# Kernel tuning notes

Hardware: AMD Instinct MI355X
Metric: run time of the kernel (lower is better)

Reference implementation:

```python
import jax, jax.numpy as jnp
import numpy as np

NQ = 11          # qubits per atom
NL = 3           # circuit layers (and message-passing layers)
S = 2 ** NQ      # statevector size
PAD = 100        # feature-map input width


def setup_inputs() -> dict:
    key = jax.random.key(0)
    ks = jax.random.split(key, 18)
    B, A, F, E = 8, 96, 64, 384
    return {
        "node_features": jax.random.normal(ks[0], (B, A, F), jnp.float32),
        "edge_indices": jax.random.randint(ks[1], (2, E), 0, A),
        # QuantumFeatureMap.feature_preprocessor: Linear(100,64) -> ReLU -> Linear(64,NQ) -> Tanh
        "W1": jax.random.normal(ks[2], (64, PAD), jnp.float32) * 0.1,
        "b1": jnp.zeros((64,), jnp.float32),
        "W2": jax.random.normal(ks[3], (NQ, 64), jnp.float32) * 0.1,
        "b2": jnp.zeros((NQ,), jnp.float32),
        # QuantumFeatureMap circuit params
        "rot": jax.random.normal(ks[4], (NL, NQ, 3), jnp.float32),
        "ent": jax.random.normal(ks[5], (NL, NQ - 1), jnp.float32),
        # one QuantumMessagePassing layer per NL, each with message_gates [NQ,3]
        "msg_gates": jax.random.normal(ks[6], (NL, NQ, 3), jnp.float32),
        # QuantumGlobalPooling
        "pool_w": jax.random.normal(ks[7], (NQ,), jnp.float32),
        # output MLP: Linear(2*NQ,256)->ReLU->Linear(256,128)->ReLU->Linear(128,64)
        "Wo1": jax.random.normal(ks[8], (256, 2 * NQ), jnp.float32) * 0.1,
        "bo1": jnp.zeros((256,), jnp.float32),
        "Wo2": jax.random.normal(ks[9], (128, 256), jnp.float32) * 0.05,
        "bo2": jnp.zeros((128,), jnp.float32),
        "Wo3": jax.random.normal(ks[10], (64, 128), jnp.float32) * 0.05,
        "bo3": jnp.zeros((64,), jnp.float32),
    }


def _apply_rotation(amps, M, q):
    """Apply per-batch 2x2 gate M [N,2,2] on qubit q of amps [N,S]."""
    N = amps.shape[0]
    lo = 1 << q
    hi = S // (2 * lo)
    a = amps.reshape(N, hi, 2, lo)  # bit q of state index is the middle axis
    return jnp.einsum('nij,nhjl->nhil', M, a).reshape(N, S)


def _forward(node_features, W1, b1, W2, b2, rot, ent, msg_gates, pool_w,
             Wo1, bo1, Wo2, bo2, Wo3, bo3):
    B, A, F = node_features.shape
    N = B * A
    # --- QuantumNodeEmbedding: pad atom features to 100, shared feature map ---
    x = node_features.reshape(N, F)
    x = jnp.pad(x, ((0, 0), (0, PAD - F)))
    h = jax.nn.relu(x @ W1.T + b1)
    f = jnp.tanh(h @ W2.T + b2)            # [N, NQ] per-qubit angles scaling
    amps = jnp.zeros((N, S), jnp.complex64).at[:, 0].set(1.0)
    states = jnp.arange(S)
    # --- QuantumFeatureMap circuit ---
    for l in range(NL):
        for q in range(NQ):
            rx = rot[l, q, 0] * f[:, q]
            ry = rot[l, q, 1] * f[:, q]
            rz = rot[l, q, 2] * f[:, q]
            cx, sx = jnp.cos(rx / 2), jnp.sin(rx / 2)
            cy, sy = jnp.cos(ry / 2), jnp.sin(ry / 2)
            cz, sz = jnp.cos(rz / 2), jnp.sin(rz / 2)
            # rotation matrix exactly as in the torch source
            M = jnp.stack([cx * cy * cz, -sx * sy * sz,
                           sx * sy * cz,  cx * cy * sz], -1)
            M = M.reshape(N, 2, 2).astype(jnp.complex64)
            amps = _apply_rotation(amps, M, q)
        for q in range(NQ - 1):
            # parameterized CNOT: for control-bit==1, mix state with target-flipped partner
            p = jax.nn.sigmoid(ent[l, q]).astype(jnp.complex64)
            ctrl = (states >> q) & 1
            partner = states ^ (1 << (q + 1))
            mixed = (1 - p) * amps + p * amps[:, partner]
            amps = jnp.where(ctrl[None, :] == 1, mixed, amps)
    # --- QuantumMessagePassing layers: diagonal phase exp(i*sum(theta_q over set bits)) ---
    bits = ((states[:, None] >> jnp.arange(NQ)[None, :]) & 1).astype(jnp.float32)  # [S,NQ]
    for l in range(NL):
        theta = msg_gates[l].sum(-1)                 # [NQ] rx+ry+rz per qubit
        phase = jnp.exp(1j * (bits @ theta))         # [S] complex64
        amps = amps * phase[None, :]
    # --- QuantumGlobalPooling ---
    amps_b = amps.reshape(B, A, S)
    w = jax.nn.sigmoid(pool_w[jnp.arange(A) % NQ]).astype(jnp.complex64)  # atom i -> w[i%NQ]
    pooled = jnp.einsum('a,bas->bs', w, amps_b)      # [B,S] complex
    norm = jnp.sqrt(jnp.sum(pooled.real ** 2 + pooled.imag ** 2, axis=1, keepdims=True))
    pooled = pooled / jnp.maximum(norm, 1e-12)
    rm = jnp.tile(pooled.real.mean(1, keepdims=True), (1, NQ))
    im = jnp.tile(pooled.imag.mean(1, keepdims=True), (1, NQ))
    rep = jnp.concatenate([rm, im], axis=1)          # [B, 2*NQ]
    # --- output network ---
    h1 = jax.nn.relu(rep @ Wo1.T + bo1)
    h2 = jax.nn.relu(h1 @ Wo2.T + bo2)
    return h2 @ Wo3.T + bo3                          # [B, 64]


def reference(node_features, edge_indices, W1, b1, W2, b2, rot, ent, msg_gates,
              pool_w, Wo1, bo1, Wo2, bo2, Wo3, bo3):
    # edge_indices is accepted by the torch module but does not enter the math
    del edge_indices
    return _forward(node_features, W1, b1, W2, b2, rot, ent, msg_gates, pool_w,
                    Wo1, bo1, Wo2, bo2, Wo3, bo3)
```

## Files before the change

kernel.cpp:

```cpp
#include <hip/hip_runtime.h>

#define NQ 11
#define NL 3
#define S  2048
#define NB 8
#define NA 96
#define NF 64
#define PADW 100
#define WPB 4
#define PPB (NA / WPB)

typedef float v2f __attribute__((ext_vector_type(2)));

#if defined(__has_builtin)
#if __has_builtin(__builtin_amdgcn_permlane16_swap) && __has_builtin(__builtin_amdgcn_permlane32_swap)
#define USE_PLSWAP 1
#endif
#endif
#ifndef USE_PLSWAP
#define USE_PLSWAP 0
#endif

__device__ __forceinline__ float sigmoidf_(float x) { return 1.0f / (1.0f + expf(-x)); }

__device__ __forceinline__ float rl_(float v, int srclane) {
    return __builtin_bit_cast(float, __builtin_amdgcn_readlane(__builtin_bit_cast(int, v), srclane));
}

template<int M> __device__ __forceinline__ float dpp_x(float x) {
    const int xi = __builtin_bit_cast(int, x);
    if constexpr (M == 1)
        return __builtin_bit_cast(float, __builtin_amdgcn_mov_dpp(xi, 0xB1, 0xF, 0xF, true));
    else if constexpr (M == 2)
        return __builtin_bit_cast(float, __builtin_amdgcn_mov_dpp(xi, 0x4E, 0xF, 0xF, true));
    else {
        static_assert(M == 8, "dpp_x: unsupported mask");
        return __builtin_bit_cast(float, __builtin_amdgcn_mov_dpp(xi, 0x128, 0xF, 0xF, true));
    }
}

__device__ __forceinline__ float dppcnd4_(float x, int lane) {
    const int xi = __builtin_bit_cast(int, x);
    const int a  = __builtin_amdgcn_mov_dpp(xi, 0x104, 0xF, 0xF, true);
    const int b  = __builtin_amdgcn_mov_dpp(xi, 0x114, 0xF, 0xF, true);
    return __builtin_bit_cast(float, (lane & 4) ? b : a);
}

template<int M> __device__ __forceinline__ void lohi_fast(float x, float& lo, float& hi) {
#if USE_PLSWAP
    const unsigned xi = __builtin_bit_cast(unsigned, x);
    if constexpr (M == 16) {
        auto p = __builtin_amdgcn_permlane16_swap(xi, xi, false, false);
        lo = __builtin_bit_cast(float, p[0]); hi = __builtin_bit_cast(float, p[1]);
    } else {
        static_assert(M == 32, "lohi_fast: unsupported mask");
        auto p = __builtin_amdgcn_permlane32_swap(xi, xi, false, false);
        lo = __builtin_bit_cast(float, p[0]); hi = __builtin_bit_cast(float, p[1]);
    }
#else
    float pw;
    int lane_ = threadIdx.x & 63;
    if constexpr (M == 16)
        pw = __builtin_bit_cast(float, __builtin_amdgcn_ds_swizzle(__builtin_bit_cast(int, x), 0x401F));
    else
        pw = __shfl_xor(x, 32, 64);
    const bool b = (lane_ & M) != 0;
    lo = b ? pw : x;
    hi = b ? x : pw;
#endif
}

template<bool FAST, int M> __device__ __forceinline__ float pxf(float x, int lane) {
    if constexpr (M == 1 || M == 2 || M == 8) {
        (void)lane; return dpp_x<M>(x);
    } else if constexpr (M == 4) {
        if constexpr (FAST) { return dppcnd4_(x, lane); }
        else { (void)lane; return __builtin_bit_cast(float,
                 __builtin_amdgcn_ds_swizzle(__builtin_bit_cast(int, x), 0x101F)); }
    } else if constexpr (M == 16) {
        if constexpr (FAST) {
            float lo, hi; lohi_fast<16>(x, lo, hi);
            return ((lane >> 4) & 1) ? lo : hi;
        } else { (void)lane; return __builtin_bit_cast(float,
                 __builtin_amdgcn_ds_swizzle(__builtin_bit_cast(int, x), 0x401F)); }
    } else {
        static_assert(M == 32, "pxf: unsupported mask");
        if constexpr (FAST) {
            float lo, hi; lohi_fast<32>(x, lo, hi);
            return ((lane >> 5) & 1) ? lo : hi;
        } else { (void)lane; return __shfl_xor(x, 32, 64); }
    }
}
template<bool FAST, int M> __device__ __forceinline__ v2f pxv(v2f w, int lane) {
    v2f r; r.x = pxf<FAST, M>(w.x, lane); r.y = pxf<FAST, M>(w.y, lane); return r;
}

template<bool FAST, int Q> __device__ __forceinline__ void rot_lane(v2f* w, float g00, float g01,
                                                                    float g10, float g11, int lane) {
    const int bit  = (lane >> Q) & 1;
    const float c1 = bit ? g11 : g00;
    const float c0 = bit ? g10 : g01;
    v2f pw[16];
#pragma unroll
    for (int j = 0; j < 16; ++j) pw[j] = pxv<FAST, (1 << Q)>(w[j], lane);
#pragma unroll
    for (int j = 0; j < 16; ++j) w[j] = c1 * w[j] + c0 * pw[j];
}
__device__ __forceinline__ void rot_comp(v2f* w, float g00, float g01, float g10, float g11) {
    v2f ca; ca.x = g00; ca.y = g11;
    v2f cb; cb.x = g01; cb.y = g10;
#pragma unroll
    for (int j = 0; j < 16; ++j) {
        v2f sw; sw.x = w[j].y; sw.y = w[j].x;
        w[j] = ca * w[j] + cb * sw;
    }
}
template<int B> __device__ __forceinline__ void rot_reg(v2f* w, float g00, float g01,
                                                        float g10, float g11) {
#pragma unroll
    for (int t = 0; t < 8; ++t) {
        const int j0 = ((t >> B) << (B + 1)) | (t & ((1 << B) - 1));
        const int j1 = j0 | (1 << B);
        v2f a0 = w[j0], a1 = w[j1];
        w[j0] = g00 * a0 + g01 * a1;
        w[j1] = g10 * a0 + g11 * a1;
    }
}
template<bool FAST, int Q> __device__ __forceinline__ void ent_lane(v2f* w, float p, int lane) {
    const float pact = p * (float)((lane >> Q) & 1);
    v2f pw[16];
#pragma unroll
    for (int j = 0; j < 16; ++j) pw[j] = pxv<FAST, (1 << (Q + 1))>(w[j], lane);
#pragma unroll
    for (int j = 0; j < 16; ++j) w[j] = w[j] + pact * (pw[j] - w[j]);
}
__device__ __forceinline__ void ent_5(v2f* w, float p, int lane) {
    const float pact = p * (float)((lane >> 5) & 1);
#pragma unroll
    for (int j = 0; j < 16; ++j) {
        v2f sw; sw.x = w[j].y; sw.y = w[j].x;
        w[j] = w[j] + pact * (sw - w[j]);
    }
}
__device__ __forceinline__ void ent_6(v2f* w, float p) {
#pragma unroll
    for (int t = 0; t < 8; ++t) {
        const int j0 = 2 * t, j1 = 2 * t + 1;
        const float d = w[j1].y - w[j0].y;
        w[j0].y = fmaf(p, d, w[j0].y);
        w[j1].y = fmaf(-p, d, w[j1].y);
    }
}
template<int B> __device__ __forceinline__ void ent_reg(v2f* w, float p) {
#pragma unroll
    for (int t = 0; t < 4; ++t) {
        const int j0 = ((t >> B) << (B + 2)) | (1 << B) | (t & ((1 << B) - 1));
        const int j1 = j0 | (1 << (B + 1));
        v2f d = w[j1] - w[j0];
        w[j0] = w[j0] + p * d;
        w[j1] = w[j1] - p * d;
    }
}

template<bool FAST> __device__ __forceinline__ void gates_run(v2f* w, float m00, float m01,
                                                              float m10, float m11, float pent,
                                                              int lane) {
#define GC(G) const int gi = gb + (G); \
    const float g00 = rl_(m00, gi), g01 = rl_(m01, gi), g10 = rl_(m10, gi), g11 = rl_(m11, gi)
#define ROTL(Q) { GC(Q); rot_lane<FAST, Q>(w, g00, g01, g10, g11, lane); }
#define ROTR(B) { GC((B) + 7); rot_reg<B>(w, g00, g01, g10, g11); }
#define ENTL(Q) { const float p = rl_(pent, eb + (Q)); ent_lane<FAST, Q>(w, p, lane); }
#pragma clang loop unroll(disable)
    for (int l = 0; l < NL; ++l) {
        const int gb = l * NQ;
        const int eb = l * (NQ - 1);
        ROTL(0) ROTL(1) ROTL(2) ROTL(3) ROTL(4) ROTL(5)
        { GC(6); rot_comp(w, g00, g01, g10, g11); }
        ROTR(0) ROTR(1) ROTR(2) ROTR(3)
        ENTL(0) ENTL(1) ENTL(2) ENTL(3) ENTL(4)
        { const float p = rl_(pent, eb + 5); ent_5(w, p, lane); }
        { const float p = rl_(pent, eb + 6); ent_6(w, p); }
        { const float p = rl_(pent, eb + 7); ent_reg<0>(w, p); }
        { const float p = rl_(pent, eb + 8); ent_reg<1>(w, p); }
        { const float p = rl_(pent, eb + 9); ent_reg<2>(w, p); }
    }
#undef GC
#undef ROTL
#undef ROTR
#undef ENTL
}

__global__ __launch_bounds__(256) void circuit_kernel(
    const float* __restrict__ nf,
    const float* __restrict__ W1,
    const float* __restrict__ b1,
    const float* __restrict__ W2,
    const float* __restrict__ b2,
    const float* __restrict__ rot,
    const float* __restrict__ ent,
    const float* __restrict__ pool_w,
    float* __restrict__ Rpart)
{
    __shared__ float W1s[64 * 65];
    __shared__ float xs[WPB][64];
    __shared__ float psum[WPB][S];

    const int tid  = threadIdx.x;
    const int lane = tid & 63;
    const int wave = tid >> 6;
    const int node = blockIdx.x * WPB + wave;
    const int a    = node % NA;

    {
        const int r  = tid >> 2;
        const int c0 = (tid & 3) << 4;
        const float4* src = reinterpret_cast<const float4*>(W1 + r * PADW + c0);
        float* dst = &W1s[r * 65 + c0];
#pragma unroll
        for (int j = 0; j < 4; ++j) {
            const float4 vv = src[j];
            dst[4 * j + 0] = vv.x; dst[4 * j + 1] = vv.y;
            dst[4 * j + 2] = vv.z; dst[4 * j + 3] = vv.w;
        }
        xs[wave][lane] = nf[blockIdx.x * (WPB * NF) + tid];
    }

    float w2v[NQ];
#pragma unroll
    for (int q = 0; q < NQ; ++q) w2v[q] = W2[q * 64 + lane];
    const float b2l = b2[lane < NQ ? lane : 0];

    bool okf;
    {
        const float idf = __builtin_bit_cast(float, lane);
        bool ok = (__builtin_bit_cast(int, dppcnd4_(idf, lane)) == (lane ^ 4));
        float lo, hi;
        lohi_fast<16>(idf, lo, hi);
        ok = ok && (__builtin_bit_cast(int, lo) == (lane & ~16))
                && (__builtin_bit_cast(int, hi) == (lane | 16));
        lohi_fast<32>(idf, lo, hi);
        ok = ok && (__builtin_bit_cast(int, lo) == (lane & ~32))
                && (__builtin_bit_cast(int, hi) == (lane | 32));
        okf = __all(ok);
    }
    __syncthreads();

    float h = b1[lane];
    {
        const float* wrow = &W1s[lane * 65];
        const float* xv   = xs[wave];
#pragma unroll
        for (int k = 0; k < 64; ++k) h = fmaf(wrow[k], xv[k], h);
    }
    h = fmaxf(h, 0.0f);

    float t[NQ];
#pragma unroll
    for (int q = 0; q < NQ; ++q) t[q] = h * w2v[q];
#pragma unroll
    for (int off = 32; off >= 1; off >>= 1) {
#pragma unroll
        for (int q = 0; q < NQ; ++q) t[q] += __shfl_xor(t[q], off, 64);
    }
    float fscal = 0.0f;
#pragma unroll
    for (int q = 0; q < NQ; ++q) if (lane == q) fscal = tanhf(t[q] + b2l);

    const int qidx = lane < 11 ? lane : (lane < 22 ? lane - 11 : (lane < 33 ? lane - 22 : 0));
    const float fg = __shfl(fscal, qidx, 64);
    float m00 = 0.f, m01 = 0.f, m10 = 0.f, m11 = 0.f;
    if (lane < NL * NQ) {
        const float* r = rot + lane * 3;
        const float hx = 0.5f * r[0] * fg;
        const float hy = 0.5f * r[1] * fg;
        const float hz = 0.5f * r[2] * fg;
        const float cx = cosf(hx), sx = sinf(hx);
        const float cy = cosf(hy), sy = sinf(hy);
        const float cz = cosf(hz), sz = sinf(hz);
        m00 = cx * cy * cz; m01 = -sx * sy * sz;
        m10 = sx * sy * cz; m11 = cx * cy * sz;
    }
    float pent = 0.0f;
    if (lane < NL * (NQ - 1)) pent = sigmoidf_(ent[lane]);

    v2f w[16];
#pragma unroll
    for (int j = 0; j < 16; ++j) { w[j].x = 0.0f; w[j].y = 0.0f; }
    if (lane == 0) w[0].x = 1.0f;

    if (okf) gates_run<true >(w, m00, m01, m10, m11, pent, lane);
    else     gates_run<false>(w, m00, m01, m10, m11, pent, lane);

    const float wgt = sigmoidf_(pool_w[a % NQ]);
#pragma unroll
    for (int j = 0; j < 16; ++j) {
        psum[wave][((2 * j + 0) << 6) | lane] = wgt * w[j].x;
        psum[wave][((2 * j + 1) << 6) | lane] = wgt * w[j].y;
    }
    __syncthreads();
    {
        float* Rb = Rpart + (size_t)blockIdx.x * S;
        for (int s = tid; s < S; s += 256)
            Rb[s] = psum[0][s] + psum[1][s] + psum[2][s] + psum[3][s];
    }
}

__global__ __launch_bounds__(512) void pool_mlp_kernel(
    const float* __restrict__ Rpart,
    const float* __restrict__ msg,
    const float* __restrict__ Wo1, const float* __restrict__ bo1,
    const float* __restrict__ Wo2, const float* __restrict__ bo2,
    const float* __restrict__ Wo3, const float* __restrict__ bo3,
    float* __restrict__ out)
{
    __shared__ float Theta[NQ];
    __shared__ float red[3][8];
    __shared__ float rm_sh, im_sh;
    __shared__ float h1[256];
    __shared__ float h2[128];

    const int b   = blockIdx.x;
    const int tid = threadIdx.x;

    if (tid < NQ) {
        float t = 0.0f;
        for (int l = 0; l < NL; ++l)
#pragma unroll
            for (int c = 0; c < 3; ++c) t += msg[(l * NQ + tid) * 3 + c];
        Theta[tid] = t;
    }
    __syncthreads();

    float psq = 0.0f, pc = 0.0f, ps = 0.0f;
    {
        const float4* Pb = reinterpret_cast<const float4*>(Rpart + (size_t)b * PPB * S);
        float4 R; R.x = 0.f; R.y = 0.f; R.z = 0.f; R.w = 0.f;
#pragma unroll 6
        for (int j = 0; j < PPB; ++j) {
            const float4 v = Pb[j * (S / 4) + tid];
            R.x += v.x; R.y += v.y; R.z += v.z; R.w += v.w;
        }
        const int s0 = tid * 4;
        float phiH = 0.0f;
#pragma unroll
        for (int q = 2; q < NQ; ++q)
            if ((s0 >> q) & 1) phiH += Theta[q];
        const float t0 = Theta[0], t1 = Theta[1];
        const float ph0 = phiH, ph1 = phiH + t0, ph2 = phiH + t1, ph3 = phiH + t0 + t1;
        psq = R.x * R.x + R.y * R.y + R.z * R.z + R.w * R.w;
        pc  = R.x * cosf(ph0) + R.y * cosf(ph1) + R.z * cosf(ph2) + R.w * cosf(ph3);
        ps  = R.x * sinf(ph0) + R.y * sinf(ph1) + R.z * sinf(ph2) + R.w * sinf(ph3);
    }
#pragma unroll
    for (int off = 32; off >= 1; off >>= 1) {
        psq += __shfl_xor(psq, off, 64);
        pc  += __shfl_xor(pc,  off, 64);
        ps  += __shfl_xor(ps,  off, 64);
    }
    const int lane = tid & 63, wave = tid >> 6;
    if (lane == 0) { red[0][wave] = psq; red[1][wave] = pc; red[2][wave] = ps; }
    __syncthreads();
    if (tid == 0) {
        float sq = 0.f, sc = 0.f, ss = 0.f;
#pragma unroll
        for (int wv = 0; wv < 8; ++wv) { sq += red[0][wv]; sc += red[1][wv]; ss += red[2][wv]; }
        const float norm = fmaxf(sqrtf(sq), 1e-12f);
        rm_sh = sc / (float)S / norm;
        im_sh = ss / (float)S / norm;
    }
    __syncthreads();
    const float rm = rm_sh, im = im_sh;

    if (tid < 256) {
        float s1 = 0.0f, s2 = 0.0f;
        const float* wrow = Wo1 + tid * (2 * NQ);
#pragma unroll
        for (int k = 0; k < NQ; ++k)       s1 += wrow[k];
#pragma unroll
        for (int k = NQ; k < 2 * NQ; ++k)  s2 += wrow[k];
        h1[tid] = fmaxf(rm * s1 + im * s2 + bo1[tid], 0.0f);
    }
    __syncthreads();
    if (tid < 128) {
        float acc = bo2[tid];
        const float* wrow = Wo2 + tid * 256;
        for (int k = 0; k < 256; ++k) acc += h1[k] * wrow[k];
        h2[tid] = fmaxf(acc, 0.0f);
    }
    __syncthreads();
    if (tid < 64) {
        float acc = bo3[tid];
        const float* wrow = Wo3 + tid * 128;
        for (int k = 0; k < 128; ++k) acc += h2[k] * wrow[k];
        out[b * 64 + tid] = acc;
    }
}

extern "C" void kernel_launch(void* const* d_in, const int* in_sizes, int n_in,
                              void* d_out, int out_size, void* d_ws, size_t ws_size,
                              hipStream_t stream) {
    const float* nf     = (const float*)d_in[0];
    const float* W1     = (const float*)d_in[2];
    const float* b1     = (const float*)d_in[3];
    const float* W2     = (const float*)d_in[4];
    const float* b2     = (const float*)d_in[5];
    const float* rot    = (const float*)d_in[6];
    const float* ent    = (const float*)d_in[7];
    const float* msg    = (const float*)d_in[8];
    const float* pool_w = (const float*)d_in[9];
    const float* Wo1    = (const float*)d_in[10];
    const float* bo1    = (const float*)d_in[11];
    const float* Wo2    = (const float*)d_in[12];
    const float* bo2    = (const float*)d_in[13];
    const float* Wo3    = (const float*)d_in[14];
    const float* bo3    = (const float*)d_in[15];

    float* Rpart = (float*)d_ws;

    circuit_kernel<<<dim3(NB * NA / WPB), dim3(256), 0, stream>>>(
        nf, W1, b1, W2, b2, rot, ent, pool_w, Rpart);

    pool_mlp_kernel<<<dim3(NB), dim3(512), 0, stream>>>(
        Rpart, msg, Wo1, bo1, Wo2, bo2, Wo3, bo3, (float*)d_out);
}
```

Baseline: 112.7 us.

## Simulate two atoms' statevectors per wave to raise per-wave ILP

Each wave now evolves two node statevectors at once, holding 32 complex pairs per lane instead of 16, so the grid halves to 96 blocks of 8 nodes. Gate coefficient readlanes and cross-lane permutes are interleaved over twice as many independent registers, which is meant to hide shuffle and FMA latency and amortise per-gate overhead. The costs are higher register pressure (launch bounds now set min blocks to 1), fewer waves in flight across the device, and a larger LDS reduction buffer per block.

```diff
diff --git a/kernel.cpp b/kernel.cpp
--- a/kernel.cpp
+++ b/kernel.cpp
@@ -8,7 +8,9 @@
 #define NF 64
 #define PADW 100
 #define WPB 4
-#define PPB (NA / WPB)
+#define NPW 2
+#define NPB (WPB * NPW)
+#define PPB (NA / NPB)
 
 typedef float v2f __attribute__((ext_vector_type(2)));
 
@@ -95,66 +97,80 @@
     v2f r; r.x = pxf<FAST, M>(w.x, lane); r.y = pxf<FAST, M>(w.y, lane); return r;
 }
 
-template<bool FAST, int Q> __device__ __forceinline__ void rot_lane(v2f* w, float g00, float g01,
-                                                                    float g10, float g11, int lane) {
-    const int bit  = (lane >> Q) & 1;
-    const float c1 = bit ? g11 : g00;
-    const float c0 = bit ? g10 : g01;
-    v2f pw[16];
-#pragma unroll
-    for (int j = 0; j < 16; ++j) pw[j] = pxv<FAST, (1 << Q)>(w[j], lane);
-#pragma unroll
-    for (int j = 0; j < 16; ++j) w[j] = c1 * w[j] + c0 * pw[j];
-}
-__device__ __forceinline__ void rot_comp(v2f* w, float g00, float g01, float g10, float g11) {
-    v2f ca; ca.x = g00; ca.y = g11;
-    v2f cb; cb.x = g01; cb.y = g10;
-#pragma unroll
-    for (int j = 0; j < 16; ++j) {
+template<bool FAST, int Q> __device__ __forceinline__ void rot_lane2(
+    v2f* w, float gA00, float gA01, float gA10, float gA11,
+            float gB00, float gB01, float gB10, float gB11, int lane) {
+    const int bit   = (lane >> Q) & 1;
+    const float cA1 = bit ? gA11 : gA00, cA0 = bit ? gA10 : gA01;
+    const float cB1 = bit ? gB11 : gB00, cB0 = bit ? gB10 : gB01;
+    v2f pw[32];
+#pragma unroll
+    for (int j = 0; j < 32; ++j) pw[j] = pxv<FAST, (1 << Q)>(w[j], lane);
+#pragma unroll
+    for (int j = 0; j < 32; ++j) {
+        const float c1 = (j < 16) ? cA1 : cB1;
+        const float c0 = (j < 16) ? cA0 : cB0;
+        w[j] = c1 * w[j] + c0 * pw[j];
+    }
+}
+__device__ __forceinline__ void rot_comp2(
+    v2f* w, float gA00, float gA01, float gA10, float gA11,
+            float gB00, float gB01, float gB10, float gB11) {
+    v2f caA; caA.x = gA00; caA.y = gA11;
+    v2f cbA; cbA.x = gA01; cbA.y = gA10;
+    v2f caB; caB.x = gB00; caB.y = gB11;
+    v2f cbB; cbB.x = gB01; cbB.y = gB10;
+#pragma unroll
+    for (int j = 0; j < 32; ++j) {
         v2f sw; sw.x = w[j].y; sw.y = w[j].x;
-        w[j] = ca * w[j] + cb * sw;
-    }
-}
-template<int B> __device__ __forceinline__ void rot_reg(v2f* w, float g00, float g01,
-                                                        float g10, float g11) {
-#pragma unroll
-    for (int t = 0; t < 8; ++t) {
-        const int j0 = ((t >> B) << (B + 1)) | (t & ((1 << B) - 1));
+        w[j] = ((j < 16) ? caA : caB) * w[j] + ((j < 16) ? cbA : cbB) * sw;
+    }
+}
+template<int B> __device__ __forceinline__ void rot_reg2(
+    v2f* w, float gA00, float gA01, float gA10, float gA11,
+            float gB00, float gB01, float gB10, float gB11) {
+#pragma unroll
+    for (int t = 0; t < 16; ++t) {
+        const int half = t >> 3, tt = t & 7;
+        const int j0 = (((tt >> B) << (B + 1)) | (tt & ((1 << B) - 1))) | (half << 4);
         const int j1 = j0 | (1 << B);
+        const float g00 = half ? gB00 : gA00, g01 = half ? gB01 : gA01;
+        const float g10 = half ? gB10 : gA10, g11 = half ? gB11 : gA11;
         v2f a0 = w[j0], a1 = w[j1];
         w[j0] = g00 * a0 + g01 * a1;
         w[j1] = g10 * a0 + g11 * a1;
     }
 }
-template<bool FAST, int Q> __device__ __forceinline__ void ent_lane(v2f* w, float p, int lane) {
+template<bool FAST, int Q> __device__ __forceinline__ void ent_lane2(v2f* w, float p, int lane) {
     const float pact = p * (float)((lane >> Q) & 1);
-    v2f pw[16];
-#pragma unroll
-    for (int j = 0; j < 16; ++j) pw[j] = pxv<FAST, (1 << (Q + 1))>(w[j], lane);
-#pragma unroll
-    for (int j = 0; j < 16; ++j) w[j] = w[j] + pact * (pw[j] - w[j]);
-}
-__device__ __forceinline__ void ent_5(v2f* w, float p, int lane) {
+    v2f pw[32];
+#pragma unroll
+    for (int j = 0; j < 32; ++j) pw[j] = pxv<FAST, (1 << (Q + 1))>(w[j], lane);
+#pragma unroll
+    for (int j = 0; j < 32; ++j) w[j] = w[j] + pact * (pw[j] - w[j]);
+}
+__device__ __forceinline__ void ent_5_2(v2f* w, float p, int lane) {
     const float pact = p * (float)((lane >> 5) & 1);
 #pragma unroll
-    for (int j = 0; j < 16; ++j) {
+    for (int j = 0; j < 32; ++j) {
         v2f sw; sw.x = w[j].y; sw.y = w[j].x;
         w[j] = w[j] + pact * (sw - w[j]);
     }
 }
-__device__ __forceinline__ void ent_6(v2f* w, float p) {
-#pragma unroll
-    for (int t = 0; t < 8; ++t) {
+__device__ __forceinline__ void ent_6_2(v2f* w, float p) {
+#pragma unroll
+    for (int t = 0; t < 16; ++t) {
         const int j0 = 2 * t, j1 = 2 * t + 1;
         const float d = w[j1].y - w[j0].y;
         w[j0].y = fmaf(p, d, w[j0].y);
         w[j1].y = fmaf(-p, d, w[j1].y);
     }
 }
-template<int B> __device__ __forceinline__ void ent_reg(v2f* w, float p) {
-#pragma unroll
-    for (int t = 0; t < 4; ++t) {
-        const int j0 = ((t >> B) << (B + 2)) | (1 << B) | (t & ((1 << B) - 1));
+template<int B> __device__ __forceinline__ void ent_reg2(v2f* w, float p) {
+#pragma unroll
+    for (int t = 0; t < 8; ++t) {
+        const int half = t >> 2, tt = t & 3;
+        const int j0 = ((((tt >> B) << (B + 2)) | (1 << B) | (tt & ((1 << B) - 1)))) | (half << 4);
         const int j1 = j0 | (1 << (B + 1));
         v2f d = w[j1] - w[j0];
         w[j0] = w[j0] + p * d;
@@ -162,35 +178,36 @@
     }
 }
 
-template<bool FAST> __device__ __forceinline__ void gates_run(v2f* w, float m00, float m01,
-                                                              float m10, float m11, float pent,
-                                                              int lane) {
-#define GC(G) const int gi = gb + (G); \
-    const float g00 = rl_(m00, gi), g01 = rl_(m01, gi), g10 = rl_(m10, gi), g11 = rl_(m11, gi)
-#define ROTL(Q) { GC(Q); rot_lane<FAST, Q>(w, g00, g01, g10, g11, lane); }
-#define ROTR(B) { GC((B) + 7); rot_reg<B>(w, g00, g01, g10, g11); }
-#define ENTL(Q) { const float p = rl_(pent, eb + (Q)); ent_lane<FAST, Q>(w, p, lane); }
+template<bool FAST> __device__ __forceinline__ void gates_run2(
+    v2f* w, float mA00, float mA01, float mA10, float mA11,
+            float mB00, float mB01, float mB10, float mB11, float pent, int lane) {
+#define GC2(G) const int gi = gb + (G); \
+    const float gA00 = rl_(mA00, gi), gA01 = rl_(mA01, gi), gA10 = rl_(mA10, gi), gA11 = rl_(mA11, gi); \
+    const float gB00 = rl_(mB00, gi), gB01 = rl_(mB01, gi), gB10 = rl_(mB10, gi), gB11 = rl_(mB11, gi)
+#define ROTL2(Q) { GC2(Q); rot_lane2<FAST, Q>(w, gA00, gA01, gA10, gA11, gB00, gB01, gB10, gB11, lane); }
+#define ROTR2(B) { GC2((B) + 7); rot_reg2<B>(w, gA00, gA01, gA10, gA11, gB00, gB01, gB10, gB11); }
+#define ENTL2(Q) { const float p = rl_(pent, eb + (Q)); ent_lane2<FAST, Q>(w, p, lane); }
 #pragma clang loop unroll(disable)
     for (int l = 0; l < NL; ++l) {
         const int gb = l * NQ;
         const int eb = l * (NQ - 1);
-        ROTL(0) ROTL(1) ROTL(2) ROTL(3) ROTL(4) ROTL(5)
-        { GC(6); rot_comp(w, g00, g01, g10, g11); }
-        ROTR(0) ROTR(1) ROTR(2) ROTR(3)
-        ENTL(0) ENTL(1) ENTL(2) ENTL(3) ENTL(4)
-        { const float p = rl_(pent, eb + 5); ent_5(w, p, lane); }
-        { const float p = rl_(pent, eb + 6); ent_6(w, p); }
-        { const float p = rl_(pent, eb + 7); ent_reg<0>(w, p); }
-        { const float p = rl_(pent, eb + 8); ent_reg<1>(w, p); }
-        { const float p = rl_(pent, eb + 9); ent_reg<2>(w, p); }
-    }
-#undef GC
-#undef ROTL
-#undef ROTR
-#undef ENTL
-}
-
-__global__ __launch_bounds__(256) void circuit_kernel(
+        ROTL2(0) ROTL2(1) ROTL2(2) ROTL2(3) ROTL2(4) ROTL2(5)
+        { GC2(6); rot_comp2(w, gA00, gA01, gA10, gA11, gB00, gB01, gB10, gB11); }
+        ROTR2(0) ROTR2(1) ROTR2(2) ROTR2(3)
+        ENTL2(0) ENTL2(1) ENTL2(2) ENTL2(3) ENTL2(4)
+        { const float p = rl_(pent, eb + 5); ent_5_2(w, p, lane); }
+        { const float p = rl_(pent, eb + 6); ent_6_2(w, p); }
+        { const float p = rl_(pent, eb + 7); ent_reg2<0>(w, p); }
+        { const float p = rl_(pent, eb + 8); ent_reg2<1>(w, p); }
+        { const float p = rl_(pent, eb + 9); ent_reg2<2>(w, p); }
+    }
+#undef GC2
+#undef ROTL2
+#undef ROTR2
+#undef ENTL2
+}
+
+__global__ __launch_bounds__(256, 1) void circuit_kernel(
     const float* __restrict__ nf,
     const float* __restrict__ W1,
     const float* __restrict__ b1,
@@ -202,14 +219,15 @@
     float* __restrict__ Rpart)
 {
     __shared__ float W1s[64 * 65];
-    __shared__ float xs[WPB][64];
-    __shared__ float psum[WPB][S];
+    __shared__ float xs[NPB][64];
+    __shared__ float psum[NPB][S];
 
     const int tid  = threadIdx.x;
     const int lane = tid & 63;
     const int wave = tid >> 6;
-    const int node = blockIdx.x * WPB + wave;
-    const int a    = node % NA;
+    const int nodeA = blockIdx.x * NPB + 2 * wave;
+    const int aA    = nodeA % NA;
+    const int aB    = (nodeA + 1) % NA;
 
     {
         const int r  = tid >> 2;
@@ -222,7 +240,10 @@
             dst[4 * j + 0] = vv.x; dst[4 * j + 1] = vv.y;
             dst[4 * j + 2] = vv.z; dst[4 * j + 3] = vv.w;
         }
-        xs[wave][lane] = nf[blockIdx.x * (WPB * NF) + tid];
+        float* xsf = &xs[0][0];
+        const int base = blockIdx.x * (NPB * NF);
+        xsf[tid]       = nf[base + tid];
+        xsf[tid + 256] = nf[base + tid + 256];
     }
 
     float w2v[NQ];
@@ -245,63 +266,91 @@
     }
     __syncthreads();
 
-    float h = b1[lane];
+    float hA = b1[lane], hB = hA;
     {
         const float* wrow = &W1s[lane * 65];
-        const float* xv   = xs[wave];
-#pragma unroll
-        for (int k = 0; k < 64; ++k) h = fmaf(wrow[k], xv[k], h);
-    }
-    h = fmaxf(h, 0.0f);
-
-    float t[NQ];
-#pragma unroll
-    for (int q = 0; q < NQ; ++q) t[q] = h * w2v[q];
+        const float* xvA  = xs[2 * wave];
+        const float* xvB  = xs[2 * wave + 1];
+#pragma unroll
+        for (int k = 0; k < 64; ++k) {
+            hA = fmaf(wrow[k], xvA[k], hA);
+            hB = fmaf(wrow[k], xvB[k], hB);
+        }
+    }
+    hA = fmaxf(hA, 0.0f);
+    hB = fmaxf(hB, 0.0f);
+
+    float tA[NQ], tB[NQ];
+#pragma unroll
+    for (int q = 0; q < NQ; ++q) { tA[q] = hA * w2v[q]; tB[q] = hB * w2v[q]; }
 #pragma unroll
     for (int off = 32; off >= 1; off >>= 1) {
 #pragma unroll
-        for (int q = 0; q < NQ; ++q) t[q] += __shfl_xor(t[q], off, 64);
-    }
-    float fscal = 0.0f;
-#pragma unroll
-    for (int q = 0; q < NQ; ++q) if (lane == q) fscal = tanhf(t[q] + b2l);
+        for (int q = 0; q < NQ; ++q) {
+            tA[q] += __shfl_xor(tA[q], off, 64);
+            tB[q] += __shfl_xor(tB[q], off, 64);
+        }
+    }
+    float fscalA = 0.0f, fscalB = 0.0f;
+#pragma unroll
+    for (int q = 0; q < NQ; ++q) {
+        if (lane == q) { fscalA = tanhf(tA[q] + b2l); fscalB = tanhf(tB[q] + b2l); }
+    }
 
     const int qidx = lane < 11 ? lane : (lane < 22 ? lane - 11 : (lane < 33 ? lane - 22 : 0));
-    const float fg = __shfl(fscal, qidx, 64);
-    float m00 = 0.f, m01 = 0.f, m10 = 0.f, m11 = 0.f;
+    const float fgA = __shfl(fscalA, qidx, 64);
+    const float fgB = __shfl(fscalB, qidx, 64);
+    float mA00 = 0.f, mA01 = 0.f, mA10 = 0.f, mA11 = 0.f;
+    float mB00 = 0.f, mB01 = 0.f, mB10 = 0.f, mB11 = 0.f;
     if (lane < NL * NQ) {
         const float* r = rot + lane * 3;
-        const float hx = 0.5f * r[0] * fg;
-        const float hy = 0.5f * r[1] * fg;
-        const float hz = 0.5f * r[2] * fg;
-        const float cx = cosf(hx), sx = sinf(hx);
-        const float cy = cosf(hy), sy = sinf(hy);
-        const float cz = cosf(hz), sz = sinf(hz);
-        m00 = cx * cy * cz; m01 = -sx * sy * sz;
-        m10 = sx * sy * cz; m11 = cx * cy * sz;
+        const float r0 = r[0], r1 = r[1], r2 = r[2];
+        {
+            const float hx = 0.5f * r0 * fgA, hy = 0.5f * r1 * fgA, hz = 0.5f * r2 * fgA;
+            const float cx = cosf(hx), sx = sinf(hx);
+            const float cy = cosf(hy), sy = sinf(hy);
+            const float cz = cosf(hz), sz = sinf(hz);
+            mA00 = cx * cy * cz; mA01 = -sx * sy * sz;
+            mA10 = sx * sy * cz; mA11 = cx * cy * sz;
+        }
+        {
+            const float hx = 0.5f * r0 * fgB, hy = 0.5f * r1 * fgB, hz = 0.5f * r2 * fgB;
+            const float cx = cosf(hx), sx = sinf(hx);
+            const float cy = cosf(hy), sy = sinf(hy);
+            const float cz = cosf(hz), sz = sinf(hz);
+            mB00 = cx * cy * cz; mB01 = -sx * sy * sz;
+            mB10 = sx * sy * cz; mB11 = cx * cy * sz;
+        }
     }
     float pent = 0.0f;
     if (lane < NL * (NQ - 1)) pent = sigmoidf_(ent[lane]);
 
-    v2f w[16];
-#pragma unroll
-    for (int j = 0; j < 16; ++j) { w[j].x = 0.0f; w[j].y = 0.0f; }
-    if (lane == 0) w[0].x = 1.0f;
-
-    if (okf) gates_run<true >(w, m00, m01, m10, m11, pent, lane);
-    else     gates_run<false>(w, m00, m01, m10, m11, pent, lane);
-
-    const float wgt = sigmoidf_(pool_w[a % NQ]);
+    v2f w[32];
+#pragma unroll
+    for (int j = 0; j < 32; ++j) { w[j].x = 0.0f; w[j].y = 0.0f; }
+    if (lane == 0) { w[0].x = 1.0f; w[16].x = 1.0f; }
+
+    if (okf) gates_run2<true >(w, mA00, mA01, mA10, mA11, mB00, mB01, mB10, mB11, pent, lane);
+    else     gates_run2<false>(w, mA00, mA01, mA10, mA11, mB00, mB01, mB10, mB11, pent, lane);
+
+    const float wgtA = sigmoidf_(pool_w[aA % NQ]);
+    const float wgtB = sigmoidf_(pool_w[aB % NQ]);
 #pragma unroll
     for (int j = 0; j < 16; ++j) {
-        psum[wave][((2 * j + 0) << 6) | lane] = wgt * w[j].x;
-        psum[wave][((2 * j + 1) << 6) | lane] = wgt * w[j].y;
+        psum[2 * wave + 0][((2 * j + 0) << 6) | lane] = wgtA * w[j].x;
+        psum[2 * wave + 0][((2 * j + 1) << 6) | lane] = wgtA * w[j].y;
+        psum[2 * wave + 1][((2 * j + 0) << 6) | lane] = wgtB * w[16 + j].x;
+        psum[2 * wave + 1][((2 * j + 1) << 6) | lane] = wgtB * w[16 + j].y;
     }
     __syncthreads();
     {
         float* Rb = Rpart + (size_t)blockIdx.x * S;
-        for (int s = tid; s < S; s += 256)
-            Rb[s] = psum[0][s] + psum[1][s] + psum[2][s] + psum[3][s];
+        for (int s = tid; s < S; s += 256) {
+            float acc = psum[0][s];
+#pragma unroll
+            for (int wv = 1; wv < NPB; ++wv) acc += psum[wv][s];
+            Rb[s] = acc;
+        }
     }
 }
 
@@ -335,7 +384,7 @@
     {
         const float4* Pb = reinterpret_cast<const float4*>(Rpart + (size_t)b * PPB * S);
         float4 R; R.x = 0.f; R.y = 0.f; R.z = 0.f; R.w = 0.f;
-#pragma unroll 6
+#pragma unroll
         for (int j = 0; j < PPB; ++j) {
             const float4 v = Pb[j * (S / 4) + tid];
             R.x += v.x; R.y += v.y; R.z += v.z; R.w += v.w;
@@ -417,7 +466,7 @@
 
     float* Rpart = (float*)d_ws;
 
-    circuit_kernel<<<dim3(NB * NA / WPB), dim3(256), 0, stream>>>(
+    circuit_kernel<<<dim3(NB * NA / NPB), dim3(256), 0, stream>>>(
         nf, W1, b1, W2, b2, rot, ent, pool_w, Rpart);
 
     pool_mlp_kernel<<<dim3(NB), dim3(512), 0, stream>>>(
```

Result: slower. 121.2 us (+7.5%).
